# Optimization experiments

Hardware: AMD Instinct MI355X
Metric: run time of the kernel (lower is better)

Reference implementation:

```python
import math
import jax, jax.numpy as jnp
import numpy as np


def _expmap0(u):
    # geoopt Lorentz (k=1) expmap0 followed by projection back onto the hyperboloid.
    # Minkowski norm of the tangent input (geoopt clamps at 1e-8 before sqrt).
    u0 = u[..., :1]
    us = u[..., 1:]
    mink = -u0 * u0 + jnp.sum(us * us, axis=-1, keepdims=True)
    nomin = jnp.sqrt(jnp.maximum(mink, 1e-8))
    r = jnp.sinh(nomin) * u / nomin
    space = r[..., 1:]
    time = jnp.sqrt(1.0 + jnp.sum(space * space, axis=-1, keepdims=True))  # project()
    return jnp.concatenate([time, space], axis=-1)


def setup_inputs() -> dict:
    key = jax.random.key(0)
    B, T, E, H = 2, 1024, 1024, 16
    ks = jax.random.split(key, 8)
    s = 0.02
    return {
        "x": jax.random.normal(ks[0], (B, T, E), jnp.float32),
        "Wqkv": jax.random.normal(ks[1], (3 * E, E), jnp.float32) * s,
        "bqkv": jnp.zeros((3 * E,), jnp.float32),
        "Wout": jax.random.normal(ks[2], (E, E), jnp.float32) * s,
        "bout": jnp.zeros((E,), jnp.float32),
        "Wimp": jax.random.normal(ks[3], (1, E), jnp.float32) * s,
        "bimp": jnp.zeros((1,), jnp.float32),
        "Walpha": jax.random.normal(ks[4], (H, E), jnp.float32) * s,
        "balpha": jnp.zeros((H,), jnp.float32),
        "spike_threshold": jnp.asarray(0.5, jnp.float32),
        "log_k": jnp.full((H,), 0.54, jnp.float32),
        "qk_scale": jnp.asarray(0.1, jnp.float32),
    }


def reference(x, Wqkv, bqkv, Wout, bout, Wimp, bimp, Walpha, balpha,
              spike_threshold, log_k, qk_scale):
    B, T, C = x.shape
    H = log_k.shape[0]
    D = C // H

    importance = jax.nn.sigmoid(x @ Wimp.T + bimp)          # (B,T,1)
    # torch.tril on the (T,1) trailing dims keeps every element -> no-op mask.
    spikes = (importance > spike_threshold).astype(x.dtype)
    spike_mask = spikes.reshape(B, 1, T, 1)

    alpha = jax.nn.sigmoid(x @ Walpha.T + balpha)           # (B,T,H)
    alpha = jnp.transpose(alpha, (0, 2, 1))[..., None]      # (B,H,T,1)

    qkv = (x @ Wqkv.T + bqkv).reshape(B, T, 3, H, D)
    q = jnp.transpose(qkv[:, :, 0], (0, 2, 1, 3))           # (B,H,T,D)
    k = jnp.transpose(qkv[:, :, 1], (0, 2, 1, 3))
    v = jnp.transpose(qkv[:, :, 2], (0, 2, 1, 3))

    scores_euclid = jnp.einsum('bhtd,bhsd->bhts', q, k) / math.sqrt(D)

    safe_scale = jax.nn.sigmoid(qk_scale) * 1.5
    qn = q / jnp.maximum(jnp.linalg.norm(q, axis=-1, keepdims=True), 1e-12) * safe_scale
    kn = k / jnp.maximum(jnp.linalg.norm(k, axis=-1, keepdims=True), 1e-12) * safe_scale
    q_hyp = _expmap0(qn)
    k_hyp = _expmap0(kn)

    inner = (-jnp.einsum('bhti,bhsi->bhts', q_hyp[..., :1], k_hyp[..., :1])
             + jnp.einsum('bhtd,bhsd->bhts', q_hyp[..., 1:], k_hyp[..., 1:]))
    curv_k = (jax.nn.softplus(log_k) + 1e-6).reshape(1, H, 1, 1)
    mdot = jnp.maximum(-inner, 1.0 + 1e-6)
    dist = jnp.arccosh(mdot)
    scores_hyper = -(dist * dist) / curv_k

    scores = (1.0 - alpha) * scores_euclid + alpha * scores_hyper
    causal = jnp.tril(jnp.ones((T, T), bool))
    scores = jnp.where(causal[None, None], scores, -jnp.inf)

    attn = jax.nn.softmax(scores, axis=-1) * spike_mask     # dropout disabled (eval)
    y = jnp.einsum('bhts,bhsd->bhtd', attn, v)
    y = jnp.transpose(y, (0, 2, 1, 3)).reshape(B, T, C)
    return y @ Wout.T + bout
```

## Files before the change

### kernel.cpp

```cpp
#include <hip/hip_runtime.h>
#include <math.h>

#define B_ 2
#define T_ 1024
#define E_ 1024
#define H_ 16
#define D_ 64
#define M_ (B_*T_)

typedef __bf16 bf16x8 __attribute__((ext_vector_type(8)));
typedef __bf16 bf16x4 __attribute__((ext_vector_type(4)));
typedef float f32x4 __attribute__((ext_vector_type(4)));

__device__ __forceinline__ void* ldsp(__bf16* base, int row, int byte) {
  return (char*)base + row * 128 + (byte ^ ((row & 7) << 4));
}

__device__ __forceinline__ void gload_lds16(const void* g, void* l) {
  __builtin_amdgcn_global_load_lds((const __attribute__((address_space(1))) void*)g,
                                   (__attribute__((address_space(3))) void*)l, 16, 0, 0);
}

#define XV4 524288
#define WQV4 786432
#define WOV4 262144
#define TOTV4 (XV4 + WQV4 + WOV4)
__global__ __launch_bounds__(256) void conv_kernel(
    const float* __restrict__ x, const float* __restrict__ Wqkv,
    const float* __restrict__ Wout,
    __bf16* __restrict__ xb, __bf16* __restrict__ Wqkvb, __bf16* __restrict__ Woutb) {
  for (size_t i = (size_t)blockIdx.x * blockDim.x + threadIdx.x; i < TOTV4;
       i += (size_t)gridDim.x * blockDim.x) {
    const float4* src; __bf16* dst; size_t off;
    if (i < XV4)            { src = (const float4*)x;    dst = xb;    off = i; }
    else if (i < XV4+WQV4)  { src = (const float4*)Wqkv; dst = Wqkvb; off = i - XV4; }
    else                    { src = (const float4*)Wout; dst = Woutb; off = i - XV4 - WQV4; }
    float4 val = src[off];
    bf16x4 o = {(__bf16)val.x, (__bf16)val.y, (__bf16)val.z, (__bf16)val.w};
    *(bf16x4*)(dst + off * 4) = o;
  }
}

__global__ __launch_bounds__(256) void imp_alpha_kernel(
    const float* __restrict__ x,
    const float* __restrict__ Wimp, const float* __restrict__ bimp,
    const float* __restrict__ Walpha, const float* __restrict__ balpha,
    const float* __restrict__ thr_p,
    float* __restrict__ spike, float* __restrict__ alpha) {
  int m = blockIdx.x;
  int tid = threadIdx.x;
  const float* xr = x + (size_t)m * E_;
  float part[17];
#pragma unroll
  for (int i = 0; i < 17; ++i) part[i] = 0.f;
  for (int e = tid; e < E_; e += 256) {
    float xv = xr[e];
    part[16] += xv * Wimp[e];
#pragma unroll
    for (int h = 0; h < 16; ++h) part[h] += xv * Walpha[h * E_ + e];
  }
  __shared__ float red[17][4];
  int lane = tid & 63, wv = tid >> 6;
#pragma unroll
  for (int i = 0; i < 17; ++i) {
    float v = part[i];
    for (int off = 32; off > 0; off >>= 1) v += __shfl_down(v, off, 64);
    if (lane == 0) red[i][wv] = v;
  }
  __syncthreads();
  if (tid < 17) {
    float v = red[tid][0] + red[tid][1] + red[tid][2] + red[tid][3];
    if (tid == 16) {
      float z = v + bimp[0];
      float sig = 1.f / (1.f + expf(-z));
      spike[m] = (sig > thr_p[0]) ? 1.f : 0.f;
    } else {
      float z = v + balpha[tid];
      float a = 1.f / (1.f + expf(-z));
      int b = m >> 10, t = m & (T_ - 1);
      alpha[((size_t)(b * H_ + tid)) * T_ + t] = a;
    }
  }
}

__global__ __launch_bounds__(256) void qkv_gemm_kernel(
    const __bf16* __restrict__ A, const __bf16* __restrict__ Bm,
    const float* __restrict__ bias,
    __bf16* __restrict__ q, __bf16* __restrict__ k, __bf16* __restrict__ v) {
  __shared__ __bf16 As[128 * 32];
  __shared__ __bf16 Bs[128 * 32];
  const int K = E_;
  int tid = threadIdx.x;
  int w = tid >> 6, lane = tid & 63, lr = lane & 15, g = lane >> 4;
  int m0 = blockIdx.y * 128, n0 = blockIdx.x * 128;
  int wr = (w >> 1) * 64, wc = (w & 1) * 64;

  int task0 = tid, task1 = tid + 256;
  int r0s = task0 >> 2, c0s = task0 & 3;
  int r1s = task1 >> 2, c1s = task1 & 3;
  const __bf16* gA0 = A + (size_t)(m0 + r0s) * K + c0s * 8;
  const __bf16* gA1 = A + (size_t)(m0 + r1s) * K + c1s * 8;
  const __bf16* gB0 = Bm + (size_t)(n0 + r0s) * K + c0s * 8;
  const __bf16* gB1 = Bm + (size_t)(n0 + r1s) * K + c1s * 8;
  __bf16* lA0 = As + task0 * 8;
  __bf16* lA1 = As + task1 * 8;
  __bf16* lB0 = Bs + task0 * 8;
  __bf16* lB1 = Bs + task1 * 8;

  f32x4 acc[4][4];
#pragma unroll
  for (int i = 0; i < 4; ++i)
#pragma unroll
    for (int j = 0; j < 4; ++j) acc[i][j] = (f32x4){0.f, 0.f, 0.f, 0.f};

  for (int k0 = 0; k0 < K; k0 += 32) {
    gload_lds16(gA0, lA0); gload_lds16(gA1, lA1);
    gload_lds16(gB0, lB0); gload_lds16(gB1, lB1);
    gA0 += 32; gA1 += 32; gB0 += 32; gB1 += 32;
    __syncthreads();
    bf16x8 af[4], bf[4];
#pragma unroll
    for (int i = 0; i < 4; ++i) af[i] = *(bf16x8*)&As[(wr + i * 16 + lr) * 32 + g * 8];
#pragma unroll
    for (int j = 0; j < 4; ++j) bf[j] = *(bf16x8*)&Bs[(wc + j * 16 + lr) * 32 + g * 8];
#pragma unroll
    for (int i = 0; i < 4; ++i)
#pragma unroll
      for (int j = 0; j < 4; ++j)
        acc[i][j] = __builtin_amdgcn_mfma_f32_16x16x32_bf16(af[i], bf[j], acc[i][j], 0, 0, 0);
    __syncthreads();
  }

#pragma unroll
  for (int i = 0; i < 4; ++i) {
#pragma unroll
    for (int r = 0; r < 4; ++r) {
      int m = m0 + wr + i * 16 + g * 4 + r;
      int b = m >> 10, t = m & (T_ - 1);
#pragma unroll
      for (int j = 0; j < 4; ++j) {
        int n = n0 + wc + j * 16 + lr;
        float val = acc[i][j][r] + bias[n];
        int comp = n >> 10, h = (n >> 6) & 15, d = n & 63;
        __bf16* dst = (comp == 0) ? q : ((comp == 1) ? k : v);
        dst[(((size_t)(b * H_ + h)) * T_ + t) * 64 + d] = (__bf16)val;
      }
    }
  }
}

__global__ __launch_bounds__(256) void hyp_kernel(
    const __bf16* __restrict__ q, const __bf16* __restrict__ k,
    const float* __restrict__ qk_scale_p,
    __bf16* __restrict__ qh, __bf16* __restrict__ khn) {
  int wid = blockIdx.x * 4 + (threadIdx.x >> 6);
  int lane = threadIdx.x & 63;
  int is_k = wid >> 15;
  int row = wid & 32767;
  const __bf16* src = (is_k ? k : q) + (size_t)row * 64;
  float u = (float)src[lane];
  float nsq = u * u;
#pragma unroll
  for (int off = 32; off > 0; off >>= 1) nsq += __shfl_xor(nsq, off, 64);
  float norm = fmaxf(sqrtf(nsq), 1e-12f);
  float ss = 1.5f / (1.f + expf(-qk_scale_p[0]));
  float un = u / norm * ss;
  float s2 = un * un;
  float tot = s2;
#pragma unroll
  for (int off = 32; off > 0; off >>= 1) tot += __shfl_xor(tot, off, 64);
  float un0 = __shfl(un, 0, 64);
  float mink = tot - 2.f * un0 * un0;
  float nomin = sqrtf(fmaxf(mink, 1e-8f));
  float sc = sinhf(nomin) / nomin;
  float r = sc * un;
  float sp2 = (lane == 0) ? 0.f : r * r;
  float sps = sp2;
#pragma unroll
  for (int off = 32; off > 0; off >>= 1) sps += __shfl_xor(sps, off, 64);
  float tm = sqrtf(1.f + sps);
  float outv = (lane == 0) ? tm : r;
  if (is_k && lane != 0) outv = -outv;
  (is_k ? khn : qh)[(size_t)row * 64 + lane] = (__bf16)outv;
}

__global__ __launch_bounds__(256) void attn_kernel(
    const __bf16* __restrict__ q, const __bf16* __restrict__ k, const __bf16* __restrict__ v,
    const __bf16* __restrict__ qh, const __bf16* __restrict__ khn,
    const float* __restrict__ alpha, const float* __restrict__ spike,
    const float* __restrict__ log_k, __bf16* __restrict__ y) {
  __shared__ __bf16 q_s[64 * 64];
  __shared__ __bf16 qh_s[64 * 64];
  __shared__ __bf16 k_s[64 * 64];
  __shared__ __bf16 kh_s[64 * 64];
  __shared__ __bf16 vt_s[64 * 64];
  __shared__ __bf16 p_s[64 * 64];

  int bid = blockIdx.x;
  int bh = bid & 31;
  int qi = 15 - (bid >> 5);
  int b = bh >> 4, h = bh & 15;
  int t0 = qi * 64;
  int tid = threadIdx.x;
  int w = tid >> 6, lane = tid & 63;
  int lr = lane & 15, g = lane >> 4;
  int trow = w * 16;
  const size_t base = (size_t)bh * T_ * 64;

#pragma unroll
  for (int it = 0; it < 2; ++it) {
    int task = tid + it * 256;
    int row = task >> 3, cj = task & 7;
    bf16x8 a = *(const bf16x8*)(q + base + (size_t)(t0 + row) * 64 + cj * 8);
    bf16x8 c = *(const bf16x8*)(qh + base + (size_t)(t0 + row) * 64 + cj * 8);
    *(bf16x8*)ldsp(q_s, row, cj * 16) = a;
    *(bf16x8*)ldsp(qh_s, row, cj * 16) = c;
  }

  float curv = log1pf(expf(log_k[h])) + 1e-6f;
  float inv_curv = 1.f / curv;
  int tg[4];
  float al[4], spv[4];
#pragma unroll
  for (int r = 0; r < 4; ++r) {
    tg[r] = t0 + trow + g * 4 + r;
    al[r] = alpha[(size_t)bh * T_ + tg[r]];
    spv[r] = spike[(size_t)b * T_ + tg[r]];
  }

  __syncthreads();
  bf16x8 aq0 = *(bf16x8*)ldsp(q_s, trow + lr, g * 16);
  bf16x8 aq1 = *(bf16x8*)ldsp(q_s, trow + lr, 64 + g * 16);
  bf16x8 ah0 = *(bf16x8*)ldsp(qh_s, trow + lr, g * 16);
  bf16x8 ah1 = *(bf16x8*)ldsp(qh_s, trow + lr, 64 + g * 16);

  float m_r[4] = {-1e30f, -1e30f, -1e30f, -1e30f};
  float l_r[4] = {0.f, 0.f, 0.f, 0.f};
  f32x4 acc[4];
#pragma unroll
  for (int n = 0; n < 4; ++n) acc[n] = (f32x4){0.f, 0.f, 0.f, 0.f};

  int ntiles = qi + 1;
  for (int st = 0; st < ntiles; ++st) {
    int s0 = st * 64;
    __syncthreads();
#pragma unroll
    for (int it = 0; it < 2; ++it) {
      int task = tid + it * 256;
      int row = task >> 3, cj = task & 7;
      bf16x8 a = *(const bf16x8*)(k + base + (size_t)(s0 + row) * 64 + cj * 8);
      bf16x8 c = *(const bf16x8*)(khn + base + (size_t)(s0 + row) * 64 + cj * 8);
      *(bf16x8*)ldsp(k_s, row, cj * 16) = a;
      *(bf16x8*)ldsp(kh_s, row, cj * 16) = c;
    }
#pragma unroll
    for (int it = 0; it < 2; ++it) {
      int task = tid + it * 256;
      int srow = task & 63, dc = task >> 6;
      bf16x8 a = *(const bf16x8*)(v + base + (size_t)(s0 + srow) * 64 + dc * 8);
#pragma unroll
      for (int i = 0; i < 8; ++i)
        *(__bf16*)ldsp(vt_s, dc * 8 + i, srow * 2) = a[i];
    }
    __syncthreads();

    f32x4 se[4], sh[4];
#pragma unroll
    for (int j = 0; j < 4; ++j) {
      bf16x8 bk0 = *(bf16x8*)ldsp(k_s, j * 16 + lr, g * 16);
      bf16x8 bk1 = *(bf16x8*)ldsp(k_s, j * 16 + lr, 64 + g * 16);
      f32x4 z = {0.f, 0.f, 0.f, 0.f};
      z = __builtin_amdgcn_mfma_f32_16x16x32_bf16(aq0, bk0, z, 0, 0, 0);
      se[j] = __builtin_amdgcn_mfma_f32_16x16x32_bf16(aq1, bk1, z, 0, 0, 0);
      bf16x8 bh0 = *(bf16x8*)ldsp(kh_s, j * 16 + lr, g * 16);
      bf16x8 bh1 = *(bf16x8*)ldsp(kh_s, j * 16 + lr, 64 + g * 16);
      f32x4 z2 = {0.f, 0.f, 0.f, 0.f};
      z2 = __builtin_amdgcn_mfma_f32_16x16x32_bf16(ah0, bh0, z2, 0, 0, 0);
      sh[j] = __builtin_amdgcn_mfma_f32_16x16x32_bf16(ah1, bh1, z2, 0, 0, 0);
    }

    float pv[4][4];
    float pmax[4] = {-1e30f, -1e30f, -1e30f, -1e30f};
#pragma unroll
    for (int j = 0; j < 4; ++j) {
      int sg = s0 + j * 16 + lr;
#pragma unroll
      for (int r = 0; r < 4; ++r) {
        float sc_e = se[j][r] * 0.125f;
        float md = fmaxf(sh[j][r], 1.0f + 1e-6f);
        float dd = __logf(md + sqrtf(md * md - 1.f));
        float s = (1.f - al[r]) * sc_e - al[r] * (dd * dd * inv_curv);
        if (sg > tg[r]) s = -1e30f;
        pv[j][r] = s;
        pmax[r] = fmaxf(pmax[r], s);
      }
    }
#pragma unroll
    for (int r = 0; r < 4; ++r) {
      float mx = pmax[r];
      mx = fmaxf(mx, __shfl_xor(mx, 1, 64));
      mx = fmaxf(mx, __shfl_xor(mx, 2, 64));
      mx = fmaxf(mx, __shfl_xor(mx, 4, 64));
      mx = fmaxf(mx, __shfl_xor(mx, 8, 64));
      float mn = fmaxf(m_r[r], mx);
      float fac = __expf(m_r[r] - mn);
      m_r[r] = mn;
      float ls = 0.f;
#pragma unroll
      for (int j = 0; j < 4; ++j) { pv[j][r] = __expf(pv[j][r] - mn); ls += pv[j][r]; }
      ls += __shfl_xor(ls, 1, 64);
      ls += __shfl_xor(ls, 2, 64);
      ls += __shfl_xor(ls, 4, 64);
      ls += __shfl_xor(ls, 8, 64);
      l_r[r] = l_r[r] * fac + ls;
#pragma unroll
      for (int n = 0; n < 4; ++n) acc[n][r] *= fac;
    }
#pragma unroll
    for (int j = 0; j < 4; ++j)
#pragma unroll
      for (int r = 0; r < 4; ++r)
        *(__bf16*)ldsp(p_s, trow + g * 4 + r, (j * 16 + lr) * 2) = (__bf16)pv[j][r];
    __syncthreads();

    bf16x8 ap0 = *(bf16x8*)ldsp(p_s, trow + lr, g * 16);
    bf16x8 ap1 = *(bf16x8*)ldsp(p_s, trow + lr, 64 + g * 16);
#pragma unroll
    for (int n = 0; n < 4; ++n) {
      bf16x8 bv0 = *(bf16x8*)ldsp(vt_s, n * 16 + lr, g * 16);
      bf16x8 bv1 = *(bf16x8*)ldsp(vt_s, n * 16 + lr, 64 + g * 16);
      acc[n] = __builtin_amdgcn_mfma_f32_16x16x32_bf16(ap0, bv0, acc[n], 0, 0, 0);
      acc[n] = __builtin_amdgcn_mfma_f32_16x16x32_bf16(ap1, bv1, acc[n], 0, 0, 0);
    }
  }

#pragma unroll
  for (int r = 0; r < 4; ++r) {
    float iv = spv[r] / l_r[r];
#pragma unroll
    for (int n = 0; n < 4; ++n) {
      y[((size_t)(b * T_ + tg[r])) * E_ + h * 64 + n * 16 + lr] =
          (__bf16)(acc[n][r] * iv);
    }
  }
}

__global__ __launch_bounds__(256) void out_gemm_kernel(
    const __bf16* __restrict__ A, const __bf16* __restrict__ Bm,
    const float* __restrict__ bias, float* __restrict__ outp) {
  __shared__ __bf16 As[128 * 32];
  __shared__ __bf16 Bs[128 * 32];
  const int K = E_;
  int tid = threadIdx.x;
  int w = tid >> 6, lane = tid & 63, lr = lane & 15, g = lane >> 4;
  int m0 = blockIdx.y * 128, n0 = blockIdx.x * 128;
  int wr = (w >> 1) * 64, wc = (w & 1) * 64;

  int task0 = tid, task1 = tid + 256;
  int r0s = task0 >> 2, c0s = task0 & 3;
  int r1s = task1 >> 2, c1s = task1 & 3;
  const __bf16* gA0 = A + (size_t)(m0 + r0s) * K + c0s * 8;
  const __bf16* gA1 = A + (size_t)(m0 + r1s) * K + c1s * 8;
  const __bf16* gB0 = Bm + (size_t)(n0 + r0s) * K + c0s * 8;
  const __bf16* gB1 = Bm + (size_t)(n0 + r1s) * K + c1s * 8;
  __bf16* lA0 = As + task0 * 8;
  __bf16* lA1 = As + task1 * 8;
  __bf16* lB0 = Bs + task0 * 8;
  __bf16* lB1 = Bs + task1 * 8;

  f32x4 acc[4][4];
#pragma unroll
  for (int i = 0; i < 4; ++i)
#pragma unroll
    for (int j = 0; j < 4; ++j) acc[i][j] = (f32x4){0.f, 0.f, 0.f, 0.f};

  for (int k0 = 0; k0 < K; k0 += 32) {
    gload_lds16(gA0, lA0); gload_lds16(gA1, lA1);
    gload_lds16(gB0, lB0); gload_lds16(gB1, lB1);
    gA0 += 32; gA1 += 32; gB0 += 32; gB1 += 32;
    __syncthreads();
    bf16x8 af[4], bf[4];
#pragma unroll
    for (int i = 0; i < 4; ++i) af[i] = *(bf16x8*)&As[(wr + i * 16 + lr) * 32 + g * 8];
#pragma unroll
    for (int j = 0; j < 4; ++j) bf[j] = *(bf16x8*)&Bs[(wc + j * 16 + lr) * 32 + g * 8];
#pragma unroll
    for (int i = 0; i < 4; ++i)
#pragma unroll
      for (int j = 0; j < 4; ++j)
        acc[i][j] = __builtin_amdgcn_mfma_f32_16x16x32_bf16(af[i], bf[j], acc[i][j], 0, 0, 0);
    __syncthreads();
  }

#pragma unroll
  for (int i = 0; i < 4; ++i) {
#pragma unroll
    for (int r = 0; r < 4; ++r) {
      int m = m0 + wr + i * 16 + g * 4 + r;
#pragma unroll
      for (int j = 0; j < 4; ++j) {
        int n = n0 + wc + j * 16 + lr;
        outp[(size_t)m * E_ + n] = acc[i][j][r] + bias[n];
      }
    }
  }
}

extern "C" void kernel_launch(void* const* d_in, const int* in_sizes, int n_in,
                              void* d_out, int out_size, void* d_ws, size_t ws_size,
                              hipStream_t stream) {
  const float* x      = (const float*)d_in[0];
  const float* Wqkv   = (const float*)d_in[1];
  const float* bqkv   = (const float*)d_in[2];
  const float* Wout   = (const float*)d_in[3];
  const float* bout   = (const float*)d_in[4];
  const float* Wimp   = (const float*)d_in[5];
  const float* bimp   = (const float*)d_in[6];
  const float* Walpha = (const float*)d_in[7];
  const float* balpha = (const float*)d_in[8];
  const float* thr    = (const float*)d_in[9];
  const float* log_k  = (const float*)d_in[10];
  const float* qk_sc  = (const float*)d_in[11];
  float* out = (float*)d_out;

  char* ws = (char*)d_ws;
  size_t off = 0;
  auto alloc = [&](size_t bytes) -> void* {
    void* p = (void*)(ws + off);
    off += (bytes + 255) & ~(size_t)255;
    return p;
  };
  const size_t qkv_elems = (size_t)B_ * H_ * T_ * D_;
  __bf16* xb    = (__bf16*)alloc((size_t)M_ * E_ * 2);
  __bf16* Wqkvb = (__bf16*)alloc((size_t)3 * E_ * E_ * 2);
  __bf16* Woutb = (__bf16*)alloc((size_t)E_ * E_ * 2);
  __bf16* q   = (__bf16*)alloc(qkv_elems * 2);
  __bf16* k   = (__bf16*)alloc(qkv_elems * 2);
  __bf16* v   = (__bf16*)alloc(qkv_elems * 2);
  __bf16* qh  = (__bf16*)alloc(qkv_elems * 2);
  __bf16* khn = (__bf16*)alloc(qkv_elems * 2);
  __bf16* yw  = (__bf16*)alloc((size_t)M_ * E_ * 2);
  float* alphaw = (float*)alloc((size_t)B_ * H_ * T_ * sizeof(float));
  float* spikew = (float*)alloc((size_t)M_ * sizeof(float));

  conv_kernel<<<1024, 256, 0, stream>>>(x, Wqkv, Wout, xb, Wqkvb, Woutb);
  imp_alpha_kernel<<<M_, 256, 0, stream>>>(x, Wimp, bimp, Walpha, balpha, thr,
                                           spikew, alphaw);
  qkv_gemm_kernel<<<dim3(24, 16), 256, 0, stream>>>(xb, Wqkvb, bqkv, q, k, v);
  hyp_kernel<<<(2 * B_ * H_ * T_) / 4, 256, 0, stream>>>(q, k, qk_sc, qh, khn);
  attn_kernel<<<B_ * H_ * (T_ / 64), 256, 0, stream>>>(q, k, v, qh, khn,
                                                       alphaw, spikew, log_k, yw);
  out_gemm_kernel<<<dim3(8, 16), 256, 0, stream>>>(yw, Woutb, bout, out);
}
```

Measured before the change: 151.9 us.

## Prefetch next K/V tile into registers, skip masked diagonal blocks, use exp2 scores

The attention kernel now loads the next K, K-hyperbolic and V tile into registers while the current tile is being processed, so global load latency overlaps with compute. Fully masked 16-column blocks on the diagonal tile skip their MFMA work, and the causal mask test runs only on that tile. Scores are rescaled into the log2 domain (folded ln2 and 1/8 constants) so exp2 and log2 replace exp and log. The block-to-query-tile mapping is reordered to interleave heavy and light causal tiles for better load balance. The register prefetch raises register pressure.

Measured after the change: 171.0 us. 1.13x slower.

```diff
diff --git a/kernel.cpp b/kernel.cpp
--- a/kernel.cpp
+++ b/kernel.cpp
@@ -197,8 +197,9 @@
   __shared__ __bf16 p_s[64 * 64];
 
   int bid = blockIdx.x;
+  int bq = bid >> 5;
+  int qi = (bq < 8) ? (15 - bq) : (bq - 8);
   int bh = bid & 31;
-  int qi = 15 - (bid >> 5);
   int b = bh >> 4, h = bh & 15;
   int t0 = qi * 64;
   int tid = threadIdx.x;
@@ -207,18 +208,26 @@
   int trow = w * 16;
   const size_t base = (size_t)bh * T_ * 64;
 
-#pragma unroll
-  for (int it = 0; it < 2; ++it) {
-    int task = tid + it * 256;
-    int row = task >> 3, cj = task & 7;
-    bf16x8 a = *(const bf16x8*)(q + base + (size_t)(t0 + row) * 64 + cj * 8);
-    bf16x8 c = *(const bf16x8*)(qh + base + (size_t)(t0 + row) * 64 + cj * 8);
-    *(bf16x8*)ldsp(q_s, row, cj * 16) = a;
-    *(bf16x8*)ldsp(qh_s, row, cj * 16) = c;
+  int task0 = tid, task1 = tid + 256;
+  int row0 = task0 >> 3, cj0 = task0 & 7;
+  int row1 = task1 >> 3, cj1 = task1 & 7;
+  int srow0 = task0 & 63, dc0 = task0 >> 6;
+  int srow1 = task1 & 63, dc1 = task1 >> 6;
+
+  {
+    bf16x8 a0 = *(const bf16x8*)(q + base + (size_t)(t0 + row0) * 64 + cj0 * 8);
+    bf16x8 c0 = *(const bf16x8*)(qh + base + (size_t)(t0 + row0) * 64 + cj0 * 8);
+    bf16x8 a1 = *(const bf16x8*)(q + base + (size_t)(t0 + row1) * 64 + cj1 * 8);
+    bf16x8 c1 = *(const bf16x8*)(qh + base + (size_t)(t0 + row1) * 64 + cj1 * 8);
+    *(bf16x8*)ldsp(q_s, row0, cj0 * 16) = a0;
+    *(bf16x8*)ldsp(qh_s, row0, cj0 * 16) = c0;
+    *(bf16x8*)ldsp(q_s, row1, cj1 * 16) = a1;
+    *(bf16x8*)ldsp(qh_s, row1, cj1 * 16) = c1;
   }
 
   float curv = log1pf(expf(log_k[h])) + 1e-6f;
-  float inv_curv = 1.f / curv;
+  float hc = 0.69314718056f / curv;
+  const float ec = 0.18033688f;
   int tg[4];
   float al[4], spv[4];
 #pragma unroll
@@ -226,6 +235,16 @@
     tg[r] = t0 + trow + g * 4 + r;
     al[r] = alpha[(size_t)bh * T_ + tg[r]];
     spv[r] = spike[(size_t)b * T_ + tg[r]];
+  }
+
+  bf16x8 rk0, rk1, rkh0, rkh1, rv0, rv1;
+  {
+    rk0  = *(const bf16x8*)(k   + base + (size_t)(row0) * 64 + cj0 * 8);
+    rkh0 = *(const bf16x8*)(khn + base + (size_t)(row0) * 64 + cj0 * 8);
+    rk1  = *(const bf16x8*)(k   + base + (size_t)(row1) * 64 + cj1 * 8);
+    rkh1 = *(const bf16x8*)(khn + base + (size_t)(row1) * 64 + cj1 * 8);
+    rv0  = *(const bf16x8*)(v   + base + (size_t)(srow0) * 64 + dc0 * 8);
+    rv1  = *(const bf16x8*)(v   + base + (size_t)(srow1) * 64 + dc1 * 8);
   }
 
   __syncthreads();
@@ -240,57 +259,58 @@
 #pragma unroll
   for (int n = 0; n < 4; ++n) acc[n] = (f32x4){0.f, 0.f, 0.f, 0.f};
 
-  int ntiles = qi + 1;
-  for (int st = 0; st < ntiles; ++st) {
+  for (int st = 0; st <= qi; ++st) {
     int s0 = st * 64;
-    __syncthreads();
-#pragma unroll
-    for (int it = 0; it < 2; ++it) {
-      int task = tid + it * 256;
-      int row = task >> 3, cj = task & 7;
-      bf16x8 a = *(const bf16x8*)(k + base + (size_t)(s0 + row) * 64 + cj * 8);
-      bf16x8 c = *(const bf16x8*)(khn + base + (size_t)(s0 + row) * 64 + cj * 8);
-      *(bf16x8*)ldsp(k_s, row, cj * 16) = a;
-      *(bf16x8*)ldsp(kh_s, row, cj * 16) = c;
-    }
-#pragma unroll
-    for (int it = 0; it < 2; ++it) {
-      int task = tid + it * 256;
-      int srow = task & 63, dc = task >> 6;
-      bf16x8 a = *(const bf16x8*)(v + base + (size_t)(s0 + srow) * 64 + dc * 8);
-#pragma unroll
-      for (int i = 0; i < 8; ++i)
-        *(__bf16*)ldsp(vt_s, dc * 8 + i, srow * 2) = a[i];
-    }
-    __syncthreads();
-
-    f32x4 se[4], sh[4];
+    bool diag = (st == qi);
+    __syncthreads();
+    *(bf16x8*)ldsp(k_s, row0, cj0 * 16) = rk0;
+    *(bf16x8*)ldsp(kh_s, row0, cj0 * 16) = rkh0;
+    *(bf16x8*)ldsp(k_s, row1, cj1 * 16) = rk1;
+    *(bf16x8*)ldsp(kh_s, row1, cj1 * 16) = rkh1;
+#pragma unroll
+    for (int i = 0; i < 8; ++i) {
+      *(__bf16*)ldsp(vt_s, dc0 * 8 + i, srow0 * 2) = rv0[i];
+      *(__bf16*)ldsp(vt_s, dc1 * 8 + i, srow1 * 2) = rv1[i];
+    }
+    if (!diag) {
+      int sn = s0 + 64;
+      rk0  = *(const bf16x8*)(k   + base + (size_t)(sn + row0) * 64 + cj0 * 8);
+      rkh0 = *(const bf16x8*)(khn + base + (size_t)(sn + row0) * 64 + cj0 * 8);
+      rk1  = *(const bf16x8*)(k   + base + (size_t)(sn + row1) * 64 + cj1 * 8);
+      rkh1 = *(const bf16x8*)(khn + base + (size_t)(sn + row1) * 64 + cj1 * 8);
+      rv0  = *(const bf16x8*)(v   + base + (size_t)(sn + srow0) * 64 + dc0 * 8);
+      rv1  = *(const bf16x8*)(v   + base + (size_t)(sn + srow1) * 64 + dc1 * 8);
+    }
+    __syncthreads();
+
+    float pv[4][4];
+    float pmax[4] = {-1e30f, -1e30f, -1e30f, -1e30f};
 #pragma unroll
     for (int j = 0; j < 4; ++j) {
+      if (diag && (s0 + j * 16 > t0 + trow + 15)) {
+#pragma unroll
+        for (int r = 0; r < 4; ++r) pv[j][r] = -1e30f;
+        continue;
+      }
       bf16x8 bk0 = *(bf16x8*)ldsp(k_s, j * 16 + lr, g * 16);
       bf16x8 bk1 = *(bf16x8*)ldsp(k_s, j * 16 + lr, 64 + g * 16);
       f32x4 z = {0.f, 0.f, 0.f, 0.f};
       z = __builtin_amdgcn_mfma_f32_16x16x32_bf16(aq0, bk0, z, 0, 0, 0);
-      se[j] = __builtin_amdgcn_mfma_f32_16x16x32_bf16(aq1, bk1, z, 0, 0, 0);
+      f32x4 se = __builtin_amdgcn_mfma_f32_16x16x32_bf16(aq1, bk1, z, 0, 0, 0);
       bf16x8 bh0 = *(bf16x8*)ldsp(kh_s, j * 16 + lr, g * 16);
       bf16x8 bh1 = *(bf16x8*)ldsp(kh_s, j * 16 + lr, 64 + g * 16);
       f32x4 z2 = {0.f, 0.f, 0.f, 0.f};
       z2 = __builtin_amdgcn_mfma_f32_16x16x32_bf16(ah0, bh0, z2, 0, 0, 0);
-      sh[j] = __builtin_amdgcn_mfma_f32_16x16x32_bf16(ah1, bh1, z2, 0, 0, 0);
-    }
-
-    float pv[4][4];
-    float pmax[4] = {-1e30f, -1e30f, -1e30f, -1e30f};
-#pragma unroll
-    for (int j = 0; j < 4; ++j) {
+      f32x4 sh = __builtin_amdgcn_mfma_f32_16x16x32_bf16(ah1, bh1, z2, 0, 0, 0);
       int sg = s0 + j * 16 + lr;
 #pragma unroll
       for (int r = 0; r < 4; ++r) {
-        float sc_e = se[j][r] * 0.125f;
-        float md = fmaxf(sh[j][r], 1.0f + 1e-6f);
-        float dd = __logf(md + sqrtf(md * md - 1.f));
-        float s = (1.f - al[r]) * sc_e - al[r] * (dd * dd * inv_curv);
-        if (sg > tg[r]) s = -1e30f;
+        float sc_e = se[r] * ec;
+        float md = fmaxf(sh[r], 1.0f + 1e-6f);
+        float l2 = __log2f(md + sqrtf(fmaf(md, md, -1.f)));
+        float t = fmaf(l2 * l2, hc, sc_e);
+        float s = fmaf(-al[r], t, sc_e);
+        if (diag && sg > tg[r]) s = -1e30f;
         pv[j][r] = s;
         pmax[r] = fmaxf(pmax[r], s);
       }
@@ -303,11 +323,11 @@
       mx = fmaxf(mx, __shfl_xor(mx, 4, 64));
       mx = fmaxf(mx, __shfl_xor(mx, 8, 64));
       float mn = fmaxf(m_r[r], mx);
-      float fac = __expf(m_r[r] - mn);
+      float fac = exp2f(m_r[r] - mn);
       m_r[r] = mn;
       float ls = 0.f;
 #pragma unroll
-      for (int j = 0; j < 4; ++j) { pv[j][r] = __expf(pv[j][r] - mn); ls += pv[j][r]; }
+      for (int j = 0; j < 4; ++j) { pv[j][r] = exp2f(pv[j][r] - mn); ls += pv[j][r]; }
       ls += __shfl_xor(ls, 1, 64);
       ls += __shfl_xor(ls, 2, 64);
       ls += __shfl_xor(ls, 4, 64);
```
